# Performance work log

Measured on AMD Instinct MI355X. Metric: run time of the kernel, lower is better.

Reference implementation:

```python
import jax, jax.numpy as jnp
import numpy as np

B, N, DQ, DK, DV = 8, 2048, 1024, 1024, 1024

def setup_inputs() -> dict:
    key = jax.random.key(0)
    kx, kq, kk, kv = jax.random.split(key, 4)
    x = jax.random.normal(kx, (B, N, DQ), dtype=jnp.float32)
    # nn.Linear(dim_q, dim_k, bias=False) weights: [out, in]
    s = 1.0 / np.sqrt(DQ)
    Wq = jax.random.uniform(kq, (DK, DQ), jnp.float32, -s, s)
    Wk = jax.random.uniform(kk, (DK, DQ), jnp.float32, -s, s)
    Wv = jax.random.uniform(kv, (DV, DQ), jnp.float32, -s, s)
    return {"x": x, "Wq": Wq, "Wk": Wk, "Wv": Wv}

def reference(x, Wq, Wk, Wv):
    batch, n, _ = x.shape
    q = jnp.einsum('bnd,kd->bnk', x, Wq)  # [B,n,DK]
    k = jnp.einsum('bnd,kd->bnk', x, Wk)  # [B,n,DK]
    v = jnp.einsum('bnd,vd->bnv', x, Wv)  # [B,n,DV]
    norm = 1.0 / jnp.sqrt(jnp.asarray(Wq.shape[0], jnp.float32))
    dist = jnp.einsum('bik,bjk->bij', q, k) * norm  # [B,n,n]
    causal = jnp.tril(jnp.ones((n, n), dtype=bool))
    dist = jnp.where(causal[None, :, :], dist, jnp.float32(-1e20))
    dist = jax.nn.softmax(dist, axis=-1)
    att = jnp.einsum('bij,bjv->biv', dist, v)  # [B,n,DV]
    return att
```

## Files before the change

### kernel.cpp

```cpp
#include <hip/hip_runtime.h>
#include <hip/hip_bf16.h>

#define BM 128
#define BN 128
#define BK 32

typedef __attribute__((ext_vector_type(4))) float floatx4;
typedef __bf16 bf16x8 __attribute__((ext_vector_type(8)));
typedef unsigned int u32;
typedef unsigned short u16;

typedef __attribute__((address_space(1))) const u32 g_u32;
typedef __attribute__((address_space(3))) u32 l_u32;

__device__ __forceinline__ u16 f32_to_bf16(float f) {
    union { float f; u32 u; } x{f};
    u32 u = x.u;
    u32 r = (u + 0x7fffu + ((u >> 16) & 1u)) >> 16;
    return (u16)r;
}

__device__ __forceinline__ float bf16_bits_to_f32(u32 hi_bits) {
    union { u32 u; float f; } x{hi_bits};
    return x.f;
}

__device__ __forceinline__ void stage_tile(const u16* gbase, int ld, u16* lds, int tid) {
#pragma unroll
    for (int it = 0; it < 2; ++it) {
        int flat = it * 2048 + tid * 8;
        int row = flat >> 5;
        int col = flat & 31;
        const u16* g = gbase + (long)row * ld + col;
        __builtin_amdgcn_global_load_lds((g_u32*)g, (l_u32*)(&lds[flat]), 16, 0, 0);
    }
}

template<bool OUT_BF16>
__device__ __forceinline__ void gemm_body(
    const u16* __restrict__ Ab, const u16* __restrict__ Bb, void* __restrict__ Cb,
    int lda, int ldb, long ldc, int m0, int n0, int nkt, float scale,
    u16* As, u16* Bs)
{
    int tid = threadIdx.x;

    stage_tile(Ab + (long)m0 * lda, lda, As, tid);
    stage_tile(Bb + (long)n0 * ldb, ldb, Bs, tid);

    int wave = tid >> 6, lane = tid & 63;
    int wr = (wave >> 1) * 64, wc = (wave & 1) * 64;
    int lrow = lane & 15, quad = lane >> 4;

    floatx4 acc[4][4] = {};
    const int aoff = (wr + lrow) * BK + quad * 8;
    const int boff = (wc + lrow) * BK + quad * 8;

    for (int kt = 0; kt < nkt; ++kt) {
        __syncthreads();
        bf16x8 af[4], bfr[4];
#pragma unroll
        for (int i = 0; i < 4; ++i) {
            af[i]  = *(const bf16x8*)&As[aoff + i * 16 * BK];
            bfr[i] = *(const bf16x8*)&Bs[boff + i * 16 * BK];
        }
#pragma unroll
        for (int mi = 0; mi < 4; ++mi)
#pragma unroll
            for (int ni = 0; ni < 4; ++ni)
                acc[mi][ni] = __builtin_amdgcn_mfma_f32_16x16x32_bf16(af[mi], bfr[ni], acc[mi][ni], 0, 0, 0);
        __syncthreads();
        if (kt + 1 < nkt) {
            stage_tile(Ab + (long)m0 * lda + (kt + 1) * BK, lda, As, tid);
            stage_tile(Bb + (long)n0 * ldb + (kt + 1) * BK, ldb, Bs, tid);
        }
    }

    long crow0 = m0 + wr + quad * 4;
    int  ccol0 = n0 + wc + lrow;
#pragma unroll
    for (int mi = 0; mi < 4; ++mi) {
#pragma unroll
        for (int ni = 0; ni < 4; ++ni) {
#pragma unroll
            for (int r = 0; r < 4; ++r) {
                long row = crow0 + mi * 16 + r;
                long col = ccol0 + ni * 16;
                float v = acc[mi][ni][r] * scale;
                if (OUT_BF16)
                    ((u16*)Cb)[row * ldc + col] = f32_to_bf16(v);
                else
                    ((float*)Cb)[row * ldc + col] = v;
            }
        }
    }
}

__global__ __launch_bounds__(256)
void qkv_gemm(const u16* __restrict__ A, const u16* __restrict__ B, u16* __restrict__ C)
{
    __shared__ u16 As[BM * BK];
    __shared__ u16 Bs[BN * BK];
    gemm_body<true>(A, B, C, 1024, 1024, 3072,
                    blockIdx.x * BM, blockIdx.y * BN, 32, 1.0f, As, Bs);
}

__global__ __launch_bounds__(256)
void s_gemm(const u16* __restrict__ QKVi, u16* __restrict__ P)
{
    __shared__ u16 As[BM * BK];
    __shared__ u16 Bs[BN * BK];
    int b = blockIdx.x, u = blockIdx.y, v = blockIdx.z;
    int mt, nt;
    if (u <= v) { mt = v; nt = u; } else { mt = 15 - v; nt = u - v - 1; }
    const u16* Ab = QKVi + (long)b * 2048 * 3072;
    const u16* Bb = Ab + 1024;
    gemm_body<true>(Ab, Bb, P + (long)b * 2048 * 2048, 3072, 3072, 2048,
                    mt * BM, nt * BN, 32, 0.03125f, As, Bs);
}

__global__ __launch_bounds__(256)
void pv_gemm(const u16* __restrict__ P, const u16* __restrict__ Vt, float* __restrict__ O)
{
    __shared__ u16 As[BM * BK];
    __shared__ u16 Bs[BN * BK];
    int b = blockIdx.x, nt = blockIdx.y, mt = blockIdx.z;
    const u16* Ab = P + (long)b * 2048 * 2048;
    const u16* Bb = Vt + (long)b * 2048;
    gemm_body<false>(Ab, Bb, O + (long)b * 2048 * 1024, 2048, 16384, 1024,
                     mt * BM, nt * BN, mt * 4 + 4, 1.0f, As, Bs);
}

__global__ __launch_bounds__(256)
void cvt_f32_bf16(const float* __restrict__ src, u16* __restrict__ dst, long n)
{
    long idx = ((long)blockIdx.x * 256 + threadIdx.x) << 2;
    if (idx >= n) return;
    float4 f = *(const float4*)(src + idx);
    ushort4 o;
    o.x = f32_to_bf16(f.x); o.y = f32_to_bf16(f.y);
    o.z = f32_to_bf16(f.z); o.w = f32_to_bf16(f.w);
    *(ushort4*)(dst + idx) = o;
}

__global__ __launch_bounds__(256)
void transpose_v(const u16* __restrict__ QKVi, u16* __restrict__ Vt)
{
    __shared__ u16 tile[64][64 + 8];
    int t0 = blockIdx.x * 64;
    int d0 = blockIdx.y * 64;
    int tid = threadIdx.x;
    int lr = tid >> 3, lc = (tid & 7) * 8;
#pragma unroll
    for (int p = 0; p < 2; ++p) {
        int tok = lr + p * 32;
        const u16* src = QKVi + (long)(t0 + tok) * 3072 + 2048 + d0 + lc;
        *(uint4*)&tile[tok][lc] = *(const uint4*)src;
    }
    __syncthreads();
#pragma unroll
    for (int p = 0; p < 2; ++p) {
        int dq = lr + p * 32;
        u16 vals[8];
#pragma unroll
        for (int i = 0; i < 8; ++i) vals[i] = tile[lc + i][dq];
        *(uint4*)(Vt + (long)(d0 + dq) * 16384 + t0 + lc) = *(const uint4*)vals;
    }
}

__global__ __launch_bounds__(256)
void softmax_causal(u16* __restrict__ P)
{
    __shared__ float red[8];
    long rowg = blockIdx.x;
    int i = (int)(rowg & 2047);
    u16* prow = P + (rowg << 11);
    int tid = threadIdx.x;
    int j0 = tid << 3;

    uint4 rv = *(const uint4*)(prow + j0);
    u32 w[4] = {rv.x, rv.y, rv.z, rv.w};
    float x[8];
#pragma unroll
    for (int t = 0; t < 4; ++t) {
        x[2 * t]     = bf16_bits_to_f32(w[t] << 16);
        x[2 * t + 1] = bf16_bits_to_f32(w[t] & 0xffff0000u);
    }
#pragma unroll
    for (int e = 0; e < 8; ++e)
        if (j0 + e > i) x[e] = -1e30f;

    float m = x[0];
#pragma unroll
    for (int e = 1; e < 8; ++e) m = fmaxf(m, x[e]);
#pragma unroll
    for (int o = 32; o; o >>= 1) m = fmaxf(m, __shfl_xor(m, o, 64));
    if ((tid & 63) == 0) red[tid >> 6] = m;
    __syncthreads();
    m = fmaxf(fmaxf(red[0], red[1]), fmaxf(red[2], red[3]));

    float e8[8], s = 0.f;
#pragma unroll
    for (int e = 0; e < 8; ++e) { e8[e] = __expf(x[e] - m); s += e8[e]; }
#pragma unroll
    for (int o = 32; o; o >>= 1) s += __shfl_xor(s, o, 64);
    if ((tid & 63) == 0) red[4 + (tid >> 6)] = s;
    __syncthreads();
    s = red[4] + red[5] + red[6] + red[7];
    float inv = 1.0f / s;

    u32 outw[4];
#pragma unroll
    for (int t = 0; t < 4; ++t) {
        u32 lo = f32_to_bf16(e8[2 * t] * inv);
        u32 hi = f32_to_bf16(e8[2 * t + 1] * inv);
        outw[t] = lo | (hi << 16);
    }
    uint4 ov; ov.x = outw[0]; ov.y = outw[1]; ov.z = outw[2]; ov.w = outw[3];
    *(uint4*)(prow + j0) = ov;
}

extern "C" void kernel_launch(void* const* d_in, const int* in_sizes, int n_in,
                              void* d_out, int out_size, void* d_ws, size_t ws_size,
                              hipStream_t stream)
{
    const int B = 8, N = 2048, D = 1024;
    const long MT = (long)B * N;
    const long nX = MT * D;
    const long nW = (long)D * D;

    const float* x  = (const float*)d_in[0];
    const float* Wq = (const float*)d_in[1];
    const float* Wk = (const float*)d_in[2];
    const float* Wv = (const float*)d_in[3];
    float* out = (float*)d_out;

    u16* wb   = (u16*)d_ws;
    u16* xb   = wb + 3 * nW;
    u16* QKVi = xb + nX;
    u16* P    = QKVi + 3 * nX;
    u16* Vt   = xb;

    cvt_f32_bf16<<<(int)(nX / 1024), 256, 0, stream>>>(x, xb, nX);
    cvt_f32_bf16<<<(int)(nW / 1024), 256, 0, stream>>>(Wq, wb, nW);
    cvt_f32_bf16<<<(int)(nW / 1024), 256, 0, stream>>>(Wk, wb + nW, nW);
    cvt_f32_bf16<<<(int)(nW / 1024), 256, 0, stream>>>(Wv, wb + 2 * nW, nW);

    qkv_gemm<<<dim3(128, 24, 1), 256, 0, stream>>>(xb, wb, QKVi);

    transpose_v<<<dim3(256, 16, 1), 256, 0, stream>>>(QKVi, Vt);

    s_gemm<<<dim3(8, 17, 8), 256, 0, stream>>>(QKVi, P);

    softmax_causal<<<(int)MT, 256, 0, stream>>>(P);

    pv_gemm<<<dim3(8, 8, 16), 256, 0, stream>>>(P, Vt, out);
}
```

Before: 429.1 us.

## Double-buffer LDS tiles in GEMM body and merge weight conversion launches

The GEMM main loop now uses two LDS buffers per operand and issues the async global-to-LDS load for the next K tile before computing on the current one. This removes one barrier per iteration and is meant to hide global load latency behind the MFMA work, at the cost of doubling LDS per block, which may reduce occupancy. Separately, the three weight conversion launches are merged into one kernel to save launch overhead.

```diff
diff --git a/kernel.cpp b/kernel.cpp
--- a/kernel.cpp
+++ b/kernel.cpp
@@ -4,6 +4,7 @@
 #define BM 128
 #define BN 128
 #define BK 32
+#define TILE_ELEMS (BM * BK)
 
 typedef __attribute__((ext_vector_type(4))) float floatx4;
 typedef __bf16 bf16x8 __attribute__((ext_vector_type(8)));
@@ -40,12 +41,17 @@
 __device__ __forceinline__ void gemm_body(
     const u16* __restrict__ Ab, const u16* __restrict__ Bb, void* __restrict__ Cb,
     int lda, int ldb, long ldc, int m0, int n0, int nkt, float scale,
-    u16* As, u16* Bs)
+    u16* smem)
 {
     int tid = threadIdx.x;
-
-    stage_tile(Ab + (long)m0 * lda, lda, As, tid);
-    stage_tile(Bb + (long)n0 * ldb, ldb, Bs, tid);
+    u16* Asb[2] = { smem,                smem + 2 * TILE_ELEMS };
+    u16* Bsb[2] = { smem + TILE_ELEMS,   smem + 3 * TILE_ELEMS };
+
+    const u16* Arow = Ab + (long)m0 * lda;
+    const u16* Brow = Bb + (long)n0 * ldb;
+
+    stage_tile(Arow, lda, Asb[0], tid);
+    stage_tile(Brow, ldb, Bsb[0], tid);
 
     int wave = tid >> 6, lane = tid & 63;
     int wr = (wave >> 1) * 64, wc = (wave & 1) * 64;
@@ -57,6 +63,13 @@
 
     for (int kt = 0; kt < nkt; ++kt) {
         __syncthreads();
+        int cur = kt & 1;
+        if (kt + 1 < nkt) {
+            stage_tile(Arow + (kt + 1) * BK, lda, Asb[cur ^ 1], tid);
+            stage_tile(Brow + (kt + 1) * BK, ldb, Bsb[cur ^ 1], tid);
+        }
+        const u16* As = Asb[cur];
+        const u16* Bs = Bsb[cur];
         bf16x8 af[4], bfr[4];
 #pragma unroll
         for (int i = 0; i < 4; ++i) {
@@ -68,11 +81,6 @@
 #pragma unroll
             for (int ni = 0; ni < 4; ++ni)
                 acc[mi][ni] = __builtin_amdgcn_mfma_f32_16x16x32_bf16(af[mi], bfr[ni], acc[mi][ni], 0, 0, 0);
-        __syncthreads();
-        if (kt + 1 < nkt) {
-            stage_tile(Ab + (long)m0 * lda + (kt + 1) * BK, lda, As, tid);
-            stage_tile(Bb + (long)n0 * ldb + (kt + 1) * BK, ldb, Bs, tid);
-        }
     }
 
     long crow0 = m0 + wr + quad * 4;
@@ -98,36 +106,33 @@
 __global__ __launch_bounds__(256)
 void qkv_gemm(const u16* __restrict__ A, const u16* __restrict__ B, u16* __restrict__ C)
 {
-    __shared__ u16 As[BM * BK];
-    __shared__ u16 Bs[BN * BK];
+    __shared__ u16 smem[4 * TILE_ELEMS];
     gemm_body<true>(A, B, C, 1024, 1024, 3072,
-                    blockIdx.x * BM, blockIdx.y * BN, 32, 1.0f, As, Bs);
+                    blockIdx.x * BM, blockIdx.y * BN, 32, 1.0f, smem);
 }
 
 __global__ __launch_bounds__(256)
 void s_gemm(const u16* __restrict__ QKVi, u16* __restrict__ P)
 {
-    __shared__ u16 As[BM * BK];
-    __shared__ u16 Bs[BN * BK];
+    __shared__ u16 smem[4 * TILE_ELEMS];
     int b = blockIdx.x, u = blockIdx.y, v = blockIdx.z;
     int mt, nt;
     if (u <= v) { mt = v; nt = u; } else { mt = 15 - v; nt = u - v - 1; }
     const u16* Ab = QKVi + (long)b * 2048 * 3072;
     const u16* Bb = Ab + 1024;
     gemm_body<true>(Ab, Bb, P + (long)b * 2048 * 2048, 3072, 3072, 2048,
-                    mt * BM, nt * BN, 32, 0.03125f, As, Bs);
+                    mt * BM, nt * BN, 32, 0.03125f, smem);
 }
 
 __global__ __launch_bounds__(256)
 void pv_gemm(const u16* __restrict__ P, const u16* __restrict__ Vt, float* __restrict__ O)
 {
-    __shared__ u16 As[BM * BK];
-    __shared__ u16 Bs[BN * BK];
+    __shared__ u16 smem[4 * TILE_ELEMS];
     int b = blockIdx.x, nt = blockIdx.y, mt = blockIdx.z;
     const u16* Ab = P + (long)b * 2048 * 2048;
     const u16* Bb = Vt + (long)b * 2048;
     gemm_body<false>(Ab, Bb, O + (long)b * 2048 * 1024, 2048, 16384, 1024,
-                     mt * BM, nt * BN, mt * 4 + 4, 1.0f, As, Bs);
+                     mt * BM, nt * BN, mt * 4 + 4, 1.0f, smem);
 }
 
 __global__ __launch_bounds__(256)
@@ -143,6 +148,20 @@
 }
 
 __global__ __launch_bounds__(256)
+void cvt_w3(const float* __restrict__ Wq, const float* __restrict__ Wk,
+            const float* __restrict__ Wv, u16* __restrict__ dst)
+{
+    int which = blockIdx.x >> 10;
+    const float* src = which == 0 ? Wq : (which == 1 ? Wk : Wv);
+    long base = (long)(blockIdx.x & 1023) * 1024 + threadIdx.x * 4;
+    float4 f = *(const float4*)(src + base);
+    ushort4 o;
+    o.x = f32_to_bf16(f.x); o.y = f32_to_bf16(f.y);
+    o.z = f32_to_bf16(f.z); o.w = f32_to_bf16(f.w);
+    *(ushort4*)(dst + (long)which * 1048576 + base) = o;
+}
+
+__global__ __launch_bounds__(256)
 void transpose_v(const u16* __restrict__ QKVi, u16* __restrict__ Vt)
 {
     __shared__ u16 tile[64][64 + 8];
@@ -241,9 +260,7 @@
     u16* Vt   = xb;
 
     cvt_f32_bf16<<<(int)(nX / 1024), 256, 0, stream>>>(x, xb, nX);
-    cvt_f32_bf16<<<(int)(nW / 1024), 256, 0, stream>>>(Wq, wb, nW);
-    cvt_f32_bf16<<<(int)(nW / 1024), 256, 0, stream>>>(Wk, wb + nW, nW);
-    cvt_f32_bf16<<<(int)(nW / 1024), 256, 0, stream>>>(Wv, wb + 2 * nW, nW);
+    cvt_w3<<<3072, 256, 0, stream>>>(Wq, Wk, Wv, wb);
 
     qkv_gemm<<<dim3(128, 24, 1), 256, 0, stream>>>(xb, wb, QKVi);
 
```

Measured after the change: 474.5 us. 10.6% more time.
